# Kernel optimization log

Measured on AMD Instinct MI355X. Metric: run time of the kernel, lower is better.

The kernel has to match this reference:

```python
import jax, jax.numpy as jnp
import numpy as np

N = 100000      # nodes
EG = 600000     # global (knn) edges used by GAT layers
E = 600000      # prediction edges scored by edge_mlp
H = 1           # gat_heads
C = 64          # hidden_dim (per-head out channels)
HC = H * C
EDGE_IN = 2 * HC + 2  # 130
EDGE_HID = EDGE_IN * 4  # 520


def gat_layer(x, W, att_src, att_dst, bias, src, dst):
    # PyG GATConv (concat=True, residual=False, no edge_dim, eval mode)
    n = x.shape[0]
    h = (x @ W).reshape(n, H, C)                      # [N,H,C]
    a_s = jnp.sum(h * att_src, axis=-1)               # [N,H]
    a_d = jnp.sum(h * att_dst, axis=-1)               # [N,H]
    alpha = jax.nn.leaky_relu(a_s[src] + a_d[dst], 0.2)  # [Eg,H]
    amax = jax.ops.segment_max(alpha, dst, num_segments=n)
    amax = jnp.where(jnp.isfinite(amax), amax, 0.0)
    e = jnp.exp(alpha - amax[dst])
    denom = jax.ops.segment_sum(e, dst, num_segments=n)
    w = e / (denom[dst] + 1e-16)                      # scatter-softmax over in-edges of dst
    out = jax.ops.segment_sum(h[src] * w[:, :, None], dst, num_segments=n)
    return out.reshape(n, HC) + bias


def setup_inputs() -> dict:
    key = jax.random.key(0)
    ks = jax.random.split(key, 16)
    glorot = lambda k, shape: jax.random.normal(k, shape, jnp.float32) * np.sqrt(2.0 / (shape[0] + shape[-1]))
    inp = {
        "pos": jax.random.normal(ks[0], (N, 3), jnp.float32),
        "edge_index": jax.random.randint(ks[1], (2, E), 0, N, jnp.int32),
        "global_edge_index": jax.random.randint(ks[2], (2, EG), 0, N, jnp.int32),
        "edge_attr": jax.random.uniform(ks[3], (E, 2), jnp.float32),
        # GAT layer 0 (in=3)
        "W0": glorot(ks[4], (3, HC)),
        "att_src0": glorot(ks[5], (1, H, C)),
        "att_dst0": glorot(ks[6], (1, H, C)),
        "b0": jnp.zeros((HC,), jnp.float32),
        # GAT layer 1 (in=HC)
        "W1": glorot(ks[7], (HC, HC)),
        "att_src1": glorot(ks[8], (1, H, C)),
        "att_dst1": glorot(ks[9], (1, H, C)),
        "b1": jnp.zeros((HC,), jnp.float32),
        # edge MLP: Linear(130,520) -> ELU -> Linear(520,1)
        "Wm1": glorot(ks[10], (EDGE_IN, EDGE_HID)),
        "bm1": jnp.zeros((EDGE_HID,), jnp.float32),
        "Wm2": glorot(ks[11], (EDGE_HID, 1)),
        "bm2": jnp.zeros((1,), jnp.float32),
    }
    return inp


def reference(pos, edge_index, global_edge_index, edge_attr,
              W0, att_src0, att_dst0, b0,
              W1, att_src1, att_dst1, b1,
              Wm1, bm1, Wm2, bm2):
    gsrc, gdst = global_edge_index[0], global_edge_index[1]
    x = pos  # dropout p=0 -> identity
    x = jax.nn.elu(gat_layer(x, W0, att_src0, att_dst0, b0, gsrc, gdst))
    x = jax.nn.elu(gat_layer(x, W1, att_src1, att_dst1, b1, gsrc, gdst))
    # per-edge gather-concat-MLP
    esrc, edst = edge_index[0], edge_index[1]
    ef = jnp.concatenate([x[esrc], x[edst], edge_attr], axis=1)  # [E, 130]
    h = jax.nn.elu(ef @ Wm1 + bm1)
    edge_values = (h @ Wm2 + bm2)[:, 0]  # [E]
    return edge_values
```

## Files before the change

kernel.cpp:

```cpp
#include <hip/hip_runtime.h>

#define KN 100000
#define KEG 600000
#define KE 600000
#define NB 98
#define LOG2E 1.4426950408889634f
#define LN2 0.6931471805599453f

#define FB_PREP 391
#define FB_CVEC 33
#define FB_HIST 2344
#define FB_T0 25000

using u16 = unsigned short;
typedef __bf16 bf16x8 __attribute__((ext_vector_type(8)));
typedef float f32x4 __attribute__((ext_vector_type(4)));
typedef float f32x2 __attribute__((ext_vector_type(2)));

__device__ __forceinline__ float b2f(u16 u) { return __uint_as_float(((unsigned)u) << 16); }
__device__ __forceinline__ u16 f2b(float f) {
  unsigned u = __float_as_uint(f);
  u += 0x7FFF + ((u >> 16) & 1);
  return (u16)(u >> 16);
}
__device__ __forceinline__ int imin(int a, int b) { return a < b ? a : b; }
__device__ __forceinline__ float fexp2(float x) {
#if __has_builtin(__builtin_amdgcn_exp2f)
  return __builtin_amdgcn_exp2f(x);
#else
  return __expf(x * LN2);
#endif
}

__device__ __forceinline__ void gload_lds16(const void* g, void* l) {
  __builtin_amdgcn_global_load_lds(
      (const __attribute__((address_space(1))) unsigned int*)g,
      (__attribute__((address_space(3))) unsigned int*)l,
      16, 0, 0);
}

__global__ __launch_bounds__(256) void k_front(
    const float* __restrict__ pos, const float* __restrict__ W0,
    const float* __restrict__ att_s, const float* __restrict__ att_d,
    const float* __restrict__ wm1, const float* __restrict__ bm1,
    const float* __restrict__ wm2, const float* __restrict__ w1,
    const int* __restrict__ gdst,
    u16* __restrict__ wm1t, u16* __restrict__ w1t, float2* __restrict__ wsc2,
    float* __restrict__ w2sum, int* __restrict__ counts, int* __restrict__ tmp_pos,
    u16* __restrict__ h, float* __restrict__ a_s, float* __restrict__ a_d) {
  int bid = blockIdx.x;
  if (bid < FB_PREP) {
    int idx = bid * 256 + threadIdx.x;
    if (idx < 33 * 5 * 512) {
      int j = idx & 7;
      int lane = (idx >> 3) & 63;
      int f = (idx >> 9) % 5;
      int nt = idx / (512 * 5);
      int n = nt * 16 + (lane & 15);
      float v = 0.f;
      if (n < 520) {
        if (f < 4) {
          int k = f * 32 + (lane >> 4) * 8 + j;
          v = wm1[k * 520 + n] * LOG2E;
        } else {
          int kk = (lane >> 4) * 8 + j;
          if (kk == 0) v = wm1[128 * 520 + n] * LOG2E;
          else if (kk == 1) v = wm1[129 * 520 + n] * LOG2E;
          else if (kk == 2) v = bm1[n] * LOG2E;
        }
      }
      wm1t[idx] = f2b(v);
    }
    if (idx < 33 * 64) {
      int lane = idx & 63, nt = idx >> 6;
      int col = nt * 16 + (lane & 15);
      float w2 = (col < 520) ? wm2[col] : 0.f;
      float2 p; p.x = w2; p.y = -LN2 * w2;
      wsc2[idx] = p;
    }
    if (idx < 4 * 2 * 64 * 8) {
      int j = idx & 7;
      int lane = (idx >> 3) & 63;
      int kt = (idx >> 9) & 1;
      int nt = idx >> 10;
      int n = nt * 16 + (lane & 15);
      int k = kt * 32 + (lane >> 4) * 8 + j;
      w1t[idx] = f2b(w1[k * 64 + n]);
    }
  } else if (bid < FB_PREP + FB_CVEC) {
    int lane = threadIdx.x & 63;
    int w = (bid - FB_PREP) * 4 + (threadIdx.x >> 6);
    float x = 0.f;
    if (w <= 129) {
      const float* row = wm1 + (size_t)w * 520;
#pragma unroll
      for (int j = 0; j < 8; ++j) x += row[j * 64 + lane] * wm2[j * 64 + lane];
      if (lane < 8) x += row[512 + lane] * wm2[512 + lane];
    } else if (w == 130) {
#pragma unroll
      for (int j = 0; j < 8; ++j) x += bm1[j * 64 + lane] * wm2[j * 64 + lane];
      if (lane < 8) x += bm1[512 + lane] * wm2[512 + lane];
    } else if (w == 131) {
#pragma unroll
      for (int j = 0; j < 8; ++j) x += wm2[j * 64 + lane];
      if (lane < 8) x += wm2[512 + lane];
    }
    for (int off = 1; off < 64; off <<= 1) x += __shfl_xor(x, off);
    if (w <= 130 && lane < 16) {
      int f = w >> 5, kk = w & 31;
      int qq = kk >> 3, jj = kk & 7;
      u16 chi = f2b(x);
      float v = (lane == 0) ? x : (lane == 1 ? (x - b2f(chi)) : 0.f);
      wm1t[(33 * 5 + f) * 512 + (qq * 16 + lane) * 8 + jj] = f2b(v);
    } else if (w == 131 && lane == 0) {
      w2sum[0] = x;
    }
  } else if (bid < FB_PREP + FB_CVEC + FB_HIST) {
    int e = (bid - (FB_PREP + FB_CVEC)) * 256 + threadIdx.x;
    if (e < KEG) tmp_pos[e] = atomicAdd(counts + gdst[e], 1);
  } else {
    int lane = threadIdx.x & 63;
    int n = (bid - (FB_PREP + FB_CVEC + FB_HIST)) * 4 + (threadIdx.x >> 6);
    float p0 = pos[n * 3 + 0], p1 = pos[n * 3 + 1], p2 = pos[n * 3 + 2];
    float hv = p0 * W0[lane] + p1 * W0[64 + lane] + p2 * W0[128 + lane];
    h[n * 64 + lane] = f2b(hv);
    float s = hv * att_s[lane];
    float d = hv * att_d[lane];
    for (int off = 1; off < 64; off <<= 1) { s += __shfl_xor(s, off); d += __shfl_xor(d, off); }
    if (lane == 0) { a_s[n] = s; a_d[n] = d; }
  }
}


__global__ __launch_bounds__(1024) void k_scan_block(
    const int* __restrict__ counts, int* __restrict__ incl, int* __restrict__ bsum) {
  int gid = blockIdx.x * 1024 + threadIdx.x;
  int lane = threadIdx.x & 63, w = threadIdx.x >> 6;
  int x = (gid < KN) ? counts[gid] : 0;
  for (int off = 1; off < 64; off <<= 1) {
    int y = __shfl_up(x, off);
    if (lane >= off) x += y;
  }
  __shared__ int wtot[16];
  if (lane == 63) wtot[w] = x;
  __syncthreads();
  if (w == 0 && lane < 16) {
    int t = wtot[lane];
    for (int off = 1; off < 16; off <<= 1) {
      int y = __shfl_up(t, off);
      if (lane >= off) t += y;
    }
    wtot[lane] = t;
  }
  __syncthreads();
  if (w > 0) x += wtot[w - 1];
  if (gid < KN) incl[gid] = x;
  if (threadIdx.x == 1023) bsum[blockIdx.x] = x;
}

__global__ __launch_bounds__(64) void k_scan_bsum(const int* __restrict__ bsum, int* __restrict__ boff) {
  int lane = threadIdx.x;
  int x0 = (lane < NB) ? bsum[lane] : 0;
  int x1 = (64 + lane < NB) ? bsum[64 + lane] : 0;
  int i0 = x0, i1 = x1;
  for (int off = 1; off < 64; off <<= 1) {
    int y0 = __shfl_up(i0, off), y1 = __shfl_up(i1, off);
    if (lane >= off) { i0 += y0; i1 += y1; }
  }
  int tot0 = __shfl(i0, 63);
  if (lane < NB) boff[lane] = i0 - x0;
  if (64 + lane < NB) boff[64 + lane] = i1 - x1 + tot0;
}

__global__ __launch_bounds__(1024) void k_scan_final(
    const int* __restrict__ incl, const int* __restrict__ counts,
    const int* __restrict__ boff, int* __restrict__ row_start) {
  int gid = blockIdx.x * 1024 + threadIdx.x;
  if (gid < KN) row_start[gid] = incl[gid] - counts[gid] + boff[blockIdx.x];
}

__global__ __launch_bounds__(256) void k_fill(
    const int* __restrict__ gsrc, const int* __restrict__ gdst,
    const int* __restrict__ row_start, const int* __restrict__ tmp_pos,
    int* __restrict__ csr_src) {
  int e = blockIdx.x * 256 + threadIdx.x;
  if (e >= KEG) return;
  int d = gdst[e];
  csr_src[row_start[d] + tmp_pos[e]] = gsrc[e];
}


__global__ __launch_bounds__(256) void k_aggt1(
    const int* __restrict__ row_start, const int* __restrict__ counts,
    const int* __restrict__ csr_src, const float* __restrict__ a_s0,
    const float* __restrict__ a_d0, const u16* __restrict__ h0,
    const float* __restrict__ b0, const u16* __restrict__ w1t,
    const float* __restrict__ as1, const float* __restrict__ ad1,
    u16* __restrict__ h1, float* __restrict__ a_s1, float* __restrict__ a_d1) {
  __shared__ u16 xb[64][72];
  int lane = threadIdx.x & 63;
  int wave = threadIdx.x >> 6;
  int nb = blockIdx.x * 64;
  int nodebase = nb + wave * 16;

  for (int i = 0; i < 16; ++i) {
    int n = nodebase + i;
    float v = 0.f;
    if (n < KN) {
      int start = row_start[n], deg = counts[n];
      float adn = a_d0[n];
      float acc = 0.f, den = 0.f;
      int j = 0;
      for (; j + 4 <= deg; j += 4) {
        int s0 = csr_src[start + j];
        int s1 = csr_src[start + j + 1];
        int s2 = csr_src[start + j + 2];
        int s3 = csr_src[start + j + 3];
        float al0 = a_s0[s0] + adn; al0 = al0 > 0.f ? al0 : 0.2f * al0;
        float al1 = a_s0[s1] + adn; al1 = al1 > 0.f ? al1 : 0.2f * al1;
        float al2 = a_s0[s2] + adn; al2 = al2 > 0.f ? al2 : 0.2f * al2;
        float al3 = a_s0[s3] + adn; al3 = al3 > 0.f ? al3 : 0.2f * al3;
        float w0 = __expf(al0), w1 = __expf(al1);
        float w2 = __expf(al2), w3 = __expf(al3);
        float h0v = b2f(h0[s0 * 64 + lane]);
        float h1v = b2f(h0[s1 * 64 + lane]);
        float h2v = b2f(h0[s2 * 64 + lane]);
        float h3v = b2f(h0[s3 * 64 + lane]);
        den += (w0 + w1) + (w2 + w3);
        acc += w0 * h0v + w1 * h1v + w2 * h2v + w3 * h3v;
      }
      for (; j < deg; ++j) {
        int s0 = csr_src[start + j];
        float al = a_s0[s0] + adn; al = al > 0.f ? al : 0.2f * al;
        float w0 = __expf(al);
        den += w0;
        acc += w0 * b2f(h0[s0 * 64 + lane]);
      }
      v = acc / (den + 1e-16f) + b0[lane];
      v = v > 0.f ? v : expm1f(v);
    }
    xb[wave * 16 + i][lane] = f2b(v);
  }

  int m = lane & 15, q = lane >> 4;
  const u16* row = xb[wave * 16 + m];
  bf16x8 A0 = *(const bf16x8*)(row + q * 8);
  bf16x8 A1 = *(const bf16x8*)(row + 32 + q * 8);

  const bf16x8* bt = (const bf16x8*)w1t;
  float ps[4] = {0.f, 0.f, 0.f, 0.f};
  float pd[4] = {0.f, 0.f, 0.f, 0.f};
#pragma unroll
  for (int nt = 0; nt < 4; ++nt) {
    int col = nt * 16 + m;
    float asv = as1[col], adv = ad1[col];
    f32x4 acc = {0.f, 0.f, 0.f, 0.f};
    acc = __builtin_amdgcn_mfma_f32_16x16x32_bf16(A0, bt[(nt * 2 + 0) * 64 + lane], acc, 0, 0, 0);
    acc = __builtin_amdgcn_mfma_f32_16x16x32_bf16(A1, bt[(nt * 2 + 1) * 64 + lane], acc, 0, 0, 0);
#pragma unroll
    for (int r = 0; r < 4; ++r) {
      int rown = nodebase + q * 4 + r;
      if (rown < KN) h1[rown * 64 + col] = f2b(acc[r]);
      ps[r] += acc[r] * asv;
      pd[r] += acc[r] * adv;
    }
  }
#pragma unroll
  for (int r = 0; r < 4; ++r) {
    float s = ps[r], d = pd[r];
    s += __shfl_xor(s, 1); d += __shfl_xor(d, 1);
    s += __shfl_xor(s, 2); d += __shfl_xor(d, 2);
    s += __shfl_xor(s, 4); d += __shfl_xor(d, 4);
    s += __shfl_xor(s, 8); d += __shfl_xor(d, 8);
    int rown = nodebase + q * 4 + r;
    if (m == 0 && rown < KN) { a_s1[rown] = s; a_d1[rown] = d; }
  }
}

__global__ __launch_bounds__(256) void k_gat_agg(
    const int* __restrict__ row_start, const int* __restrict__ counts,
    const int* __restrict__ csr_src, const float* __restrict__ a_s,
    const float* __restrict__ a_d, const u16* __restrict__ h,
    const float* __restrict__ bias, u16* __restrict__ xout) {
  int lane = threadIdx.x & 63;
  int n = blockIdx.x * 4 + (threadIdx.x >> 6);
  int start = row_start[n], deg = counts[n];
  float adn = a_d[n];
  float acc = 0.f, den = 0.f;
  int j = 0;
  for (; j + 4 <= deg; j += 4) {
    int s0 = csr_src[start + j];
    int s1 = csr_src[start + j + 1];
    int s2 = csr_src[start + j + 2];
    int s3 = csr_src[start + j + 3];
    float al0 = a_s[s0] + adn; al0 = al0 > 0.f ? al0 : 0.2f * al0;
    float al1 = a_s[s1] + adn; al1 = al1 > 0.f ? al1 : 0.2f * al1;
    float al2 = a_s[s2] + adn; al2 = al2 > 0.f ? al2 : 0.2f * al2;
    float al3 = a_s[s3] + adn; al3 = al3 > 0.f ? al3 : 0.2f * al3;
    float w0 = __expf(al0), w1 = __expf(al1);
    float w2 = __expf(al2), w3 = __expf(al3);
    float h0 = b2f(h[s0 * 64 + lane]);
    float h1 = b2f(h[s1 * 64 + lane]);
    float h2 = b2f(h[s2 * 64 + lane]);
    float h3 = b2f(h[s3 * 64 + lane]);
    den += (w0 + w1) + (w2 + w3);
    acc += w0 * h0 + w1 * h1 + w2 * h2 + w3 * h3;
  }
  for (; j < deg; ++j) {
    int s0 = csr_src[start + j];
    float al = a_s[s0] + adn; al = al > 0.f ? al : 0.2f * al;
    float w0 = __expf(al);
    den += w0;
    acc += w0 * b2f(h[s0 * 64 + lane]);
  }
  float v = acc / (den + 1e-16f) + bias[lane];
  v = v > 0.f ? v : expm1f(v);
  xout[n * 64 + lane] = f2b(v);
}

__global__ __launch_bounds__(256) void k_edge_mlp(
    const int* __restrict__ eidx, const u16* __restrict__ x2bf,
    const float* __restrict__ eattr, const u16* __restrict__ wm1t,
    const float2* __restrict__ wsc2, const float* __restrict__ w2sum,
    const float* __restrict__ bm2, float* __restrict__ out) {
  __shared__ uint4 Bbuf[2][1408];
  int tid = threadIdx.x;
  int lane = tid & 63;
  int wave = tid >> 6;
  int base = blockIdx.x * 256 + wave * 64;
  int m = lane & 15, q = lane >> 4;

  bf16x8 A[4][4];
#pragma unroll
  for (int s = 0; s < 4; ++s) {
    int row = imin(base + s * 16 + m, KE - 1);
    int es = eidx[row], ed = eidx[KE + row];
    const bf16x8* psrc = (const bf16x8*)(x2bf + es * 64);
    const bf16x8* pdst = (const bf16x8*)(x2bf + ed * 64);
    A[s][0] = psrc[q];
    A[s][1] = psrc[q + 4];
    A[s][2] = pdst[q];
    A[s][3] = pdst[q + 4];
  }
  bf16x8 A5[4];
#pragma unroll
  for (int s = 0; s < 4; ++s) {
    bf16x8 a5 = {0, 0, 0, 0, 0, 0, 0, 0};
    if (q == 0) {
      int row = imin(base + s * 16 + m, KE - 1);
      a5[0] = (__bf16)eattr[row * 2 + 0];
      a5[1] = (__bf16)eattr[row * 2 + 1];
      a5[2] = (__bf16)1.0f;
    }
    A5[s] = a5;
  }

  const uint4* gB = (const uint4*)wm1t;
  const uint4* gW = (const uint4*)wsc2;
#pragma unroll
  for (int k = 0; k < 5; ++k)
    gload_lds16(gB + tid + k * 256, &Bbuf[0][tid + k * 256]);
  gload_lds16(gW + lane, &Bbuf[0][1280 + lane]);
  gload_lds16(gW + 64 + lane, &Bbuf[0][1280 + 64 + lane]);

  f32x2 osum[4][2];
#pragma unroll
  for (int s = 0; s < 4; ++s) {
    osum[s][0] = (f32x2){0.f, 0.f};
    osum[s][1] = (f32x2){0.f, 0.f};
  }

#pragma unroll 1
  for (int ch = 0; ch < 9; ++ch) {
    int cur = ch & 1, nxt = cur ^ 1;
    if (ch > 0) __builtin_amdgcn_s_barrier();
    if (ch < 8) {
      const uint4* gs = gB + (ch + 1) * 1280;
#pragma unroll
      for (int k = 0; k < 5; ++k)
        gload_lds16(gs + tid + k * 256, &Bbuf[nxt][tid + k * 256]);
      const uint4* ws = gW + (ch + 1) * 128;
      gload_lds16(ws + lane, &Bbuf[nxt][1280 + lane]);
      gload_lds16(ws + 64 + lane, &Bbuf[nxt][1280 + 64 + lane]);
      asm volatile("s_waitcnt vmcnt(7)" ::: "memory");
    } else {
      asm volatile("s_waitcnt vmcnt(0)" ::: "memory");
    }
    __builtin_amdgcn_s_barrier();

    int lim = (ch == 8) ? 1 : 4;
#pragma unroll 1
    for (int li = 0; li < lim; ++li) {
      const bf16x8* lb = (const bf16x8*)(Bbuf[cur] + li * 5 * 64);
      bf16x8 B0 = lb[0 * 64 + lane];
      bf16x8 B1 = lb[1 * 64 + lane];
      bf16x8 B2 = lb[2 * 64 + lane];
      bf16x8 B3 = lb[3 * 64 + lane];
      bf16x8 B4 = lb[4 * 64 + lane];
      float2 w2 = ((const float2*)(Bbuf[cur] + 1280))[li * 64 + lane];
#pragma unroll
      for (int s = 0; s < 4; ++s) {
        f32x4 acc = {0.f, 0.f, 0.f, 0.f};
        acc = __builtin_amdgcn_mfma_f32_16x16x32_bf16(A[s][0], B0, acc, 0, 0, 0);
        acc = __builtin_amdgcn_mfma_f32_16x16x32_bf16(A[s][1], B1, acc, 0, 0, 0);
        acc = __builtin_amdgcn_mfma_f32_16x16x32_bf16(A[s][2], B2, acc, 0, 0, 0);
        acc = __builtin_amdgcn_mfma_f32_16x16x32_bf16(A[s][3], B3, acc, 0, 0, 0);
        acc = __builtin_amdgcn_mfma_f32_16x16x32_bf16(A5[s],   B4, acc, 0, 0, 0);
        f32x2 t0 = {fminf(acc[0], 0.f), fminf(acc[1], 0.f)};
        f32x2 t1 = {fminf(acc[2], 0.f), fminf(acc[3], 0.f)};
        f32x2 e0 = {fexp2(t0.x), fexp2(t0.y)};
        f32x2 e1 = {fexp2(t1.x), fexp2(t1.y)};
        osum[s][0] += e0 * w2.x + t0 * w2.y;
        osum[s][1] += e1 * w2.x + t1 * w2.y;
      }
    }
  }

  const bf16x8* bt = (const bf16x8*)wm1t;
  bf16x8 L0 = bt[(33 * 5 + 0) * 64 + lane];
  bf16x8 L1 = bt[(33 * 5 + 1) * 64 + lane];
  bf16x8 L2 = bt[(33 * 5 + 2) * 64 + lane];
  bf16x8 L3 = bt[(33 * 5 + 3) * 64 + lane];
  bf16x8 L4 = bt[(33 * 5 + 4) * 64 + lane];
  float w2s = w2sum[0];
  float b2v = bm2[0];

#pragma unroll
  for (int s = 0; s < 4; ++s) {
    f32x4 accL = {0.f, 0.f, 0.f, 0.f};
    accL = __builtin_amdgcn_mfma_f32_16x16x32_bf16(A[s][0], L0, accL, 0, 0, 0);
    accL = __builtin_amdgcn_mfma_f32_16x16x32_bf16(A[s][1], L1, accL, 0, 0, 0);
    accL = __builtin_amdgcn_mfma_f32_16x16x32_bf16(A[s][2], L2, accL, 0, 0, 0);
    accL = __builtin_amdgcn_mfma_f32_16x16x32_bf16(A[s][3], L3, accL, 0, 0, 0);
    accL = __builtin_amdgcn_mfma_f32_16x16x32_bf16(A5[s],   L4, accL, 0, 0, 0);
    float ov[4] = {osum[s][0].x, osum[s][0].y, osum[s][1].x, osum[s][1].y};
#pragma unroll
    for (int r = 0; r < 4; ++r) {
      float lin = accL[r] + __shfl_xor(accL[r], 1);
      float v = ov[r];
      v += __shfl_xor(v, 1);
      v += __shfl_xor(v, 2);
      v += __shfl_xor(v, 4);
      v += __shfl_xor(v, 8);
      if (m == 0) {
        int row = base + s * 16 + q * 4 + r;
        if (row < KE) out[row] = v - w2s + lin + b2v;
      }
    }
  }
}

extern "C" void kernel_launch(void* const* d_in, const int* in_sizes, int n_in,
                              void* d_out, int out_size, void* d_ws, size_t ws_size,
                              hipStream_t stream) {
  const float* pos  = (const float*)d_in[0];
  const int* eidx   = (const int*)d_in[1];
  const int* geidx  = (const int*)d_in[2];
  const float* eattr= (const float*)d_in[3];
  const float* W0   = (const float*)d_in[4];
  const float* as0  = (const float*)d_in[5];
  const float* ad0  = (const float*)d_in[6];
  const float* b0   = (const float*)d_in[7];
  const float* W1   = (const float*)d_in[8];
  const float* as1  = (const float*)d_in[9];
  const float* ad1  = (const float*)d_in[10];
  const float* b1   = (const float*)d_in[11];
  const float* Wm1  = (const float*)d_in[12];
  const float* bm1  = (const float*)d_in[13];
  const float* Wm2  = (const float*)d_in[14];
  const float* bm2  = (const float*)d_in[15];
  float* out = (float*)d_out;

  char* ws = (char*)d_ws;
  size_t off = 0;
  auto carve = [&](size_t bytes) {
    char* p = ws + off;
    off = (off + bytes + 255) & ~(size_t)255;
    return p;
  };
  int* counts    = (int*)carve((size_t)KN * 4);
  int* incl      = (int*)carve((size_t)KN * 4);
  int* row_start = (int*)carve((size_t)KN * 4);
  int* bsum      = (int*)carve(128 * 4);
  int* boff      = (int*)carve(128 * 4);
  int* csr_src   = (int*)carve((size_t)KEG * 4);
  int* tmp_pos   = (int*)carve((size_t)KEG * 4);
  u16* h0        = (u16*)carve((size_t)KN * 64 * 2);
  u16* h1        = (u16*)carve((size_t)KN * 64 * 2);
  u16* x12       = (u16*)carve((size_t)KN * 64 * 2);
  float* a_s0    = (float*)carve((size_t)KN * 4);
  float* a_d0    = (float*)carve((size_t)KN * 4);
  float* a_s1    = (float*)carve((size_t)KN * 4);
  float* a_d1    = (float*)carve((size_t)KN * 4);
  u16* wm1t      = (u16*)carve((size_t)36 * 5 * 512 * 2);
  u16* w1t       = (u16*)carve((size_t)4 * 2 * 64 * 8 * 2);
  float2* wsc2   = (float2*)carve((size_t)36 * 64 * 8);
  float* w2sum   = (float*)carve(256);

  const int* gsrc = geidx;
  const int* gdst = geidx + KEG;

  hipMemsetAsync(d_ws, 0, (size_t)KN * 4, stream);

  k_front<<<FB_PREP + FB_CVEC + FB_HIST + FB_T0, 256, 0, stream>>>(
      pos, W0, as0, ad0, Wm1, bm1, Wm2, W1, gdst,
      wm1t, w1t, wsc2, w2sum, counts, tmp_pos, h0, a_s0, a_d0);

  k_scan_block<<<NB, 1024, 0, stream>>>(counts, incl, bsum);
  k_scan_bsum<<<1, 64, 0, stream>>>(bsum, boff);
  k_scan_final<<<NB, 1024, 0, stream>>>(incl, counts, boff, row_start);
  k_fill<<<(KEG + 255) / 256, 256, 0, stream>>>(gsrc, gdst, row_start, tmp_pos, csr_src);

  k_aggt1<<<(KN + 63) / 64, 256, 0, stream>>>(row_start, counts, csr_src,
                                              a_s0, a_d0, h0, b0,
                                              w1t, as1, ad1, h1, a_s1, a_d1);

  k_gat_agg<<<KN / 4, 256, 0, stream>>>(row_start, counts, csr_src, a_s1, a_d1, h1, b1, x12);

  k_edge_mlp<<<(KE + 255) / 256, 256, 0, stream>>>(eidx, x12, eattr, wm1t, wsc2, w2sum, bm2, out);
}
```

Baseline: 361.2 us.

## Shrink aggt1 to 16 nodes per block and dedupe redundant weight loads in edge MLP

k_aggt1 now handles 16 nodes per block (4 per wave) instead of 64, raising the block count from about 1563 to 6250. Each wave computes one 16-column slice of the 64x64 layer-1 transform with MFMA. Partial attention dot products are combined across waves through shared memory. In k_edge_mlp, only wave 3 issues the second-layer weight copies into LDS instead of all four waves writing the same data, with adjusted vmcnt waits. The cost is extra __syncthreads and an LDS reduction step. Bounds checks are dropped, which relies on KN being divisible by 16.

```diff
diff --git a/kernel.cpp b/kernel.cpp
--- a/kernel.cpp
+++ b/kernel.cpp
@@ -197,83 +197,91 @@
     const float* __restrict__ b0, const u16* __restrict__ w1t,
     const float* __restrict__ as1, const float* __restrict__ ad1,
     u16* __restrict__ h1, float* __restrict__ a_s1, float* __restrict__ a_d1) {
-  __shared__ u16 xb[64][72];
+  __shared__ u16 xb[16][72];
+  __shared__ float psum[2][4][16];
   int lane = threadIdx.x & 63;
   int wave = threadIdx.x >> 6;
-  int nb = blockIdx.x * 64;
-  int nodebase = nb + wave * 16;
-
-  for (int i = 0; i < 16; ++i) {
-    int n = nodebase + i;
-    float v = 0.f;
-    if (n < KN) {
-      int start = row_start[n], deg = counts[n];
-      float adn = a_d0[n];
-      float acc = 0.f, den = 0.f;
-      int j = 0;
-      for (; j + 4 <= deg; j += 4) {
-        int s0 = csr_src[start + j];
-        int s1 = csr_src[start + j + 1];
-        int s2 = csr_src[start + j + 2];
-        int s3 = csr_src[start + j + 3];
-        float al0 = a_s0[s0] + adn; al0 = al0 > 0.f ? al0 : 0.2f * al0;
-        float al1 = a_s0[s1] + adn; al1 = al1 > 0.f ? al1 : 0.2f * al1;
-        float al2 = a_s0[s2] + adn; al2 = al2 > 0.f ? al2 : 0.2f * al2;
-        float al3 = a_s0[s3] + adn; al3 = al3 > 0.f ? al3 : 0.2f * al3;
-        float w0 = __expf(al0), w1 = __expf(al1);
-        float w2 = __expf(al2), w3 = __expf(al3);
-        float h0v = b2f(h0[s0 * 64 + lane]);
-        float h1v = b2f(h0[s1 * 64 + lane]);
-        float h2v = b2f(h0[s2 * 64 + lane]);
-        float h3v = b2f(h0[s3 * 64 + lane]);
-        den += (w0 + w1) + (w2 + w3);
-        acc += w0 * h0v + w1 * h1v + w2 * h2v + w3 * h3v;
-      }
-      for (; j < deg; ++j) {
-        int s0 = csr_src[start + j];
-        float al = a_s0[s0] + adn; al = al > 0.f ? al : 0.2f * al;
-        float w0 = __expf(al);
-        den += w0;
-        acc += w0 * b2f(h0[s0 * 64 + lane]);
-      }
-      v = acc / (den + 1e-16f) + b0[lane];
-      v = v > 0.f ? v : expm1f(v);
-    }
-    xb[wave * 16 + i][lane] = f2b(v);
-  }
+  int nodebase = blockIdx.x * 16;
+
+  int st0 = row_start[nodebase + wave * 4 + 0];
+  int st1 = row_start[nodebase + wave * 4 + 1];
+  int st2 = row_start[nodebase + wave * 4 + 2];
+  int st3 = row_start[nodebase + wave * 4 + 3];
+  int dg0 = counts[nodebase + wave * 4 + 0];
+  int dg1 = counts[nodebase + wave * 4 + 1];
+  int dg2 = counts[nodebase + wave * 4 + 2];
+  int dg3 = counts[nodebase + wave * 4 + 3];
+  float adn0 = a_d0[nodebase + wave * 4 + 0];
+  float adn1 = a_d0[nodebase + wave * 4 + 1];
+  float adn2 = a_d0[nodebase + wave * 4 + 2];
+  float adn3 = a_d0[nodebase + wave * 4 + 3];
+#pragma unroll
+  for (int i = 0; i < 4; ++i) {
+    int start = i == 0 ? st0 : (i == 1 ? st1 : (i == 2 ? st2 : st3));
+    int deg   = i == 0 ? dg0 : (i == 1 ? dg1 : (i == 2 ? dg2 : dg3));
+    float adn = i == 0 ? adn0 : (i == 1 ? adn1 : (i == 2 ? adn2 : adn3));
+    float acc = 0.f, den = 0.f;
+    int j = 0;
+    for (; j + 4 <= deg; j += 4) {
+      int s0 = csr_src[start + j];
+      int s1 = csr_src[start + j + 1];
+      int s2 = csr_src[start + j + 2];
+      int s3 = csr_src[start + j + 3];
+      float al0 = a_s0[s0] + adn; al0 = al0 > 0.f ? al0 : 0.2f * al0;
+      float al1 = a_s0[s1] + adn; al1 = al1 > 0.f ? al1 : 0.2f * al1;
+      float al2 = a_s0[s2] + adn; al2 = al2 > 0.f ? al2 : 0.2f * al2;
+      float al3 = a_s0[s3] + adn; al3 = al3 > 0.f ? al3 : 0.2f * al3;
+      float w0 = __expf(al0), w1 = __expf(al1);
+      float w2 = __expf(al2), w3 = __expf(al3);
+      float h0v = b2f(h0[s0 * 64 + lane]);
+      float h1v = b2f(h0[s1 * 64 + lane]);
+      float h2v = b2f(h0[s2 * 64 + lane]);
+      float h3v = b2f(h0[s3 * 64 + lane]);
+      den += (w0 + w1) + (w2 + w3);
+      acc += w0 * h0v + w1 * h1v + w2 * h2v + w3 * h3v;
+    }
+    for (; j < deg; ++j) {
+      int s0 = csr_src[start + j];
+      float al = a_s0[s0] + adn; al = al > 0.f ? al : 0.2f * al;
+      float w0 = __expf(al);
+      den += w0;
+      acc += w0 * b2f(h0[s0 * 64 + lane]);
+    }
+    float v = acc / (den + 1e-16f) + b0[lane];
+    v = v > 0.f ? v : expm1f(v);
+    xb[wave * 4 + i][lane] = f2b(v);
+  }
+  __syncthreads();
 
   int m = lane & 15, q = lane >> 4;
-  const u16* row = xb[wave * 16 + m];
+  const u16* row = xb[m];
   bf16x8 A0 = *(const bf16x8*)(row + q * 8);
   bf16x8 A1 = *(const bf16x8*)(row + 32 + q * 8);
 
   const bf16x8* bt = (const bf16x8*)w1t;
-  float ps[4] = {0.f, 0.f, 0.f, 0.f};
-  float pd[4] = {0.f, 0.f, 0.f, 0.f};
-#pragma unroll
-  for (int nt = 0; nt < 4; ++nt) {
-    int col = nt * 16 + m;
-    float asv = as1[col], adv = ad1[col];
-    f32x4 acc = {0.f, 0.f, 0.f, 0.f};
-    acc = __builtin_amdgcn_mfma_f32_16x16x32_bf16(A0, bt[(nt * 2 + 0) * 64 + lane], acc, 0, 0, 0);
-    acc = __builtin_amdgcn_mfma_f32_16x16x32_bf16(A1, bt[(nt * 2 + 1) * 64 + lane], acc, 0, 0, 0);
-#pragma unroll
-    for (int r = 0; r < 4; ++r) {
-      int rown = nodebase + q * 4 + r;
-      if (rown < KN) h1[rown * 64 + col] = f2b(acc[r]);
-      ps[r] += acc[r] * asv;
-      pd[r] += acc[r] * adv;
-    }
-  }
+  int nt = wave;
+  int col = nt * 16 + m;
+  float asv = as1[col], adv = ad1[col];
+  f32x4 acc = {0.f, 0.f, 0.f, 0.f};
+  acc = __builtin_amdgcn_mfma_f32_16x16x32_bf16(A0, bt[(nt * 2 + 0) * 64 + lane], acc, 0, 0, 0);
+  acc = __builtin_amdgcn_mfma_f32_16x16x32_bf16(A1, bt[(nt * 2 + 1) * 64 + lane], acc, 0, 0, 0);
 #pragma unroll
   for (int r = 0; r < 4; ++r) {
-    float s = ps[r], d = pd[r];
+    int rown = nodebase + q * 4 + r;
+    h1[rown * 64 + col] = f2b(acc[r]);
+    float s = acc[r] * asv, d = acc[r] * adv;
     s += __shfl_xor(s, 1); d += __shfl_xor(d, 1);
     s += __shfl_xor(s, 2); d += __shfl_xor(d, 2);
     s += __shfl_xor(s, 4); d += __shfl_xor(d, 4);
     s += __shfl_xor(s, 8); d += __shfl_xor(d, 8);
-    int rown = nodebase + q * 4 + r;
-    if (m == 0 && rown < KN) { a_s1[rown] = s; a_d1[rown] = d; }
+    if (m == 0) { psum[0][wave][q * 4 + r] = s; psum[1][wave][q * 4 + r] = d; }
+  }
+  __syncthreads();
+
+  if (threadIdx.x < 16) {
+    int i = threadIdx.x;
+    a_s1[nodebase + i] = psum[0][0][i] + psum[0][1][i] + psum[0][2][i] + psum[0][3][i];
+    a_d1[nodebase + i] = psum[1][0][i] + psum[1][1][i] + psum[1][2][i] + psum[1][3][i];
   }
 }
 
@@ -360,8 +368,10 @@
 #pragma unroll
   for (int k = 0; k < 5; ++k)
     gload_lds16(gB + tid + k * 256, &Bbuf[0][tid + k * 256]);
-  gload_lds16(gW + lane, &Bbuf[0][1280 + lane]);
-  gload_lds16(gW + 64 + lane, &Bbuf[0][1280 + 64 + lane]);
+  if (wave == 3) {
+    gload_lds16(gW + lane, &Bbuf[0][1280 + lane]);
+    gload_lds16(gW + 64 + lane, &Bbuf[0][1280 + 64 + lane]);
+  }
 
   f32x2 osum[4][2];
 #pragma unroll
@@ -379,10 +389,14 @@
 #pragma unroll
       for (int k = 0; k < 5; ++k)
         gload_lds16(gs + tid + k * 256, &Bbuf[nxt][tid + k * 256]);
-      const uint4* ws = gW + (ch + 1) * 128;
-      gload_lds16(ws + lane, &Bbuf[nxt][1280 + lane]);
-      gload_lds16(ws + 64 + lane, &Bbuf[nxt][1280 + 64 + lane]);
-      asm volatile("s_waitcnt vmcnt(7)" ::: "memory");
+      if (wave == 3) {
+        const uint4* ws = gW + (ch + 1) * 128;
+        gload_lds16(ws + lane, &Bbuf[nxt][1280 + lane]);
+        gload_lds16(ws + 64 + lane, &Bbuf[nxt][1280 + 64 + lane]);
+        asm volatile("s_waitcnt vmcnt(7)" ::: "memory");
+      } else {
+        asm volatile("s_waitcnt vmcnt(5)" ::: "memory");
+      }
     } else {
       asm volatile("s_waitcnt vmcnt(0)" ::: "memory");
     }
@@ -511,9 +525,9 @@
   k_scan_final<<<NB, 1024, 0, stream>>>(incl, counts, boff, row_start);
   k_fill<<<(KEG + 255) / 256, 256, 0, stream>>>(gsrc, gdst, row_start, tmp_pos, csr_src);
 
-  k_aggt1<<<(KN + 63) / 64, 256, 0, stream>>>(row_start, counts, csr_src,
-                                              a_s0, a_d0, h0, b0,
-                                              w1t, as1, ad1, h1, a_s1, a_d1);
+  k_aggt1<<<KN / 16, 256, 0, stream>>>(row_start, counts, csr_src,
+                                       a_s0, a_d0, h0, b0,
+                                       w1t, as1, ad1, h1, a_s1, a_d1);
 
   k_gat_agg<<<KN / 4, 256, 0, stream>>>(row_start, counts, csr_src, a_s1, a_d1, h1, b1, x12);
 
```

Measured after the change: 354.8 us. No clear change (-1.8%).
